# Kernel optimization log

Measured on AMD Instinct MI355X. Metric: run time of the kernel, lower is better.

Reference implementation:

```python
import jax, jax.numpy as jnp
import numpy as np
from jax import lax

DN = ('NCHW', 'OIHW', 'NCHW')

def _conv(x, w, b):
    y = lax.conv_general_dilated(x, w, (1, 1), 'SAME', dimension_numbers=DN)
    return y + b[None, :, None, None]

def setup_inputs() -> dict:
    key = jax.random.key(0)
    ks = jax.random.split(key, 12)
    B, C, H, W = 8, 32, 128, 128
    Cb, INT, K, FK = 64, 64, 3, 3
    inp = {
        'z': jax.random.normal(ks[0], (B, C, H, W), jnp.float32),
        'backbone': jax.random.normal(ks[1], (B, Cb, H, W), jnp.float32),
        'mem_stab': jax.random.normal(ks[2], (B, C, H, W), jnp.float32),
        'mem_unstab': jax.random.normal(ks[3], (B, C, H, W), jnp.float32),
        'w0': jax.random.normal(ks[4], (INT, Cb + 3 * C, K, K), jnp.float32) * 0.05,
        'b0': jnp.zeros((INT,), jnp.float32),
        'w1': jax.random.normal(ks[5], (INT, INT, K, K), jnp.float32) * 0.05,
        'b1': jnp.zeros((INT,), jnp.float32),
        'w2': jax.random.normal(ks[6], (INT, INT, K, K), jnp.float32) * 0.05,
        'b2': jnp.zeros((INT,), jnp.float32),
        'w_last': jax.random.normal(ks[7], (C * FK * FK, INT, K, K), jnp.float32) * 0.05,
        'b_last': jnp.full((C * FK * FK,), -4.0, jnp.float32),
        'fusion_kernel_size': FK,
    }
    return inp

def reference(z, backbone, mem_stab, mem_unstab, w0, b0, w1, b1, w2, b2, w_last, b_last, fusion_kernel_size):
    B, C, H, W = z.shape
    k = int(fusion_kernel_size)
    p = k * k
    # controller conv stack (LeakyReLU slope 0.01, matching nn.LeakyReLU default)
    q = jnp.concatenate([backbone, z, mem_stab, mem_unstab], axis=1)
    q = jax.nn.leaky_relu(_conv(q, w0, b0), 0.01)
    q = jax.nn.leaky_relu(_conv(q, w1, b1), 0.01)
    q = jax.nn.leaky_relu(_conv(q, w2, b2), 0.01)
    # fusion head -> [B, C, p, HW]
    head = _conv(q, w_last, b_last).reshape(B, C, p, H * W)
    # softmax over p kernel positions + one extra logit-0 slot for z itself
    eta = jax.nn.softmax(jnp.concatenate([head, jnp.zeros_like(head[:, :, :1])], axis=2), axis=2)
    # unfold(mem_stab, k, padding=k//2): patches ordered (c, kh, kw) like torch unfold
    pad = k // 2
    mpad = jnp.pad(mem_stab, ((0, 0), (0, 0), (pad, pad), (pad, pad)))
    patches = jnp.stack([mpad[:, :, i:i + H, j:j + W] for i in range(k) for j in range(k)], axis=2)
    patches = patches.reshape(B, C, p, H * W)
    z_flat = z.reshape(B, C, H * W)
    z_stab = (patches * eta[:, :, :p]).sum(axis=2) + eta[:, :, p] * z_flat
    return z_stab.reshape(B, C, H, W)
```

## Files before the change

kernel.cpp:

```cpp
#include <hip/hip_runtime.h>
#include <hip/hip_fp16.h>

typedef _Float16 half8 __attribute__((ext_vector_type(8)));
typedef _Float16 half4v __attribute__((ext_vector_type(4)));
typedef float floatx4 __attribute__((ext_vector_type(4)));

#define HW 128
#define IMG (HW * HW)
#define PH 130
#define WP 200

typedef __attribute__((address_space(3))) _Float16 lds_f16;
typedef __attribute__((address_space(1))) const _Float16 glb_f16;
__device__ __forceinline__ void gload16(const _Float16* g, _Float16* l) {
    __builtin_amdgcn_global_load_lds((glb_f16*)g, (lds_f16*)l, 16, 0, 0);
}

__global__ void pack_w_all(const float* __restrict__ w0, const float* __restrict__ w1,
                           const float* __restrict__ w2, const float* __restrict__ wl,
                           _Float16* __restrict__ p0, _Float16* __restrict__ p1,
                           _Float16* __restrict__ p2, _Float16* __restrict__ pl) {
    int idx = blockIdx.x * 256 + threadIdx.x;
    const float* w; _Float16* p; int C; int local;
    if (idx < 92160)       { w = w0; p = p0; C = 160; local = idx; }
    else if (idx < 129024) { w = w1; p = p1; C = 64;  local = idx - 92160; }
    else if (idx < 165888) { w = w2; p = p2; C = 64;  local = idx - 129024; }
    else if (idx < 331776) { w = wl; p = pl; C = 64;  local = idx - 165888; }
    else return;
    int o = local / (C * 9);
    int rem = local % (C * 9);
    int c = rem / 9;
    int t = rem % 9;
    p[(o * 9 + t) * C + c] = (_Float16)w[local];
}

__device__ __forceinline__ void zero_halo(_Float16* P, int C, int id) {
    int nvec = C / 8;
    int b = id / (516 * nvec);
    int r = id % (516 * nvec);
    int cell = r / nvec;
    int v = r % nvec;
    int hh, ww;
    if (cell < 130)      { hh = 0;   ww = cell; }
    else if (cell < 260) { hh = 129; ww = cell - 130; }
    else if (cell < 388) { hh = cell - 260 + 1; ww = 0; }
    else                 { hh = cell - 388 + 1; ww = 129; }
    half8 z8 = {};
    *reinterpret_cast<half8*>(P + (((size_t)b * PH + hh) * PH + ww) * C + v * 8) = z8;
}

__global__ void zero_pads_pre(_Float16* __restrict__ X0, _Float16* __restrict__ Q1) {
    int id = blockIdx.x * 256 + threadIdx.x;
    if (id < 82560) zero_halo(X0, 160, id);
    else if (id < 115584) zero_halo(Q1, 64, id - 82560);
}

__global__ void zero_pads64(_Float16* __restrict__ P) {
    int id = blockIdx.x * 256 + threadIdx.x;
    if (id < 33024) zero_halo(P, 64, id);
}

__global__ __launch_bounds__(256)
void pack_in(const float* __restrict__ z, const float* __restrict__ bb,
             const float* __restrict__ ms, const float* __restrict__ mu,
             _Float16* __restrict__ X0) {
    __shared__ _Float16 lds[160 * 132];
    int b = blockIdx.x >> 7;
    int h = blockIdx.x & 127;
    int tid = threadIdx.x;

    for (int i = 0; i < 20; i++) {
        int id = i * 256 + tid;
        int c = id >> 5;
        int col = (id & 31) * 4;
        const float* src; int cs; int csz;
        if (c < 64)       { src = bb; cs = c;       csz = 64; }
        else if (c < 96)  { src = z;  cs = c - 64;  csz = 32; }
        else if (c < 128) { src = ms; cs = c - 96;  csz = 32; }
        else              { src = mu; cs = c - 128; csz = 32; }
        float4 v = *reinterpret_cast<const float4*>(
            src + ((size_t)b * csz + cs) * IMG + h * HW + col);
        half4v hv = { (_Float16)v.x, (_Float16)v.y, (_Float16)v.z, (_Float16)v.w };
        *reinterpret_cast<half4v*>(&lds[c * 132 + col]) = hv;
    }
    __syncthreads();
    _Float16* dst = X0 + (((size_t)b * PH + (h + 1)) * PH + 1) * 160;
    for (int i = 0; i < 10; i++) {
        int id = i * 256 + tid;
        int pix = id / 20;
        int c0 = (id % 20) * 8;
        half8 hv;
        #pragma unroll
        for (int e = 0; e < 8; e++) hv[e] = lds[(c0 + e) * 132 + pix];
        *reinterpret_cast<half8*>(dst + (size_t)pix * 160 + c0) = hv;
    }
}

__global__ __launch_bounds__(256, 2)
void conv3_c160(const _Float16* __restrict__ X, const _Float16* __restrict__ Wp,
                const float* __restrict__ bias, _Float16* __restrict__ Y) {
    __shared__ _Float16 xs[130 * 168];
    int b = blockIdx.x >> 7;
    int h = blockIdx.x & 127;
    int tid = threadIdx.x;
    int lane = tid & 63;
    int wave = tid >> 6;
    int ph = wave & 1;
    int oh = wave >> 1;
    int l15 = lane & 15;
    int l4  = lane >> 4;

    floatx4 acc[4][2] = {};
    half8 SA[10], SB[10];

    const _Float16* wl = Wp + (size_t)((oh * 32 + l15) * 9) * 160 + l4 * 8;

#define LOADW(S, k) { \
    _Pragma("unroll") \
    for (int cb = 0; cb < 5; cb++) \
      _Pragma("unroll") \
      for (int n = 0; n < 2; n++) \
        S[cb * 2 + n] = *reinterpret_cast<const half8*>( \
            wl + n * 23040 + (k) * 160 + cb * 32); }

#define STAGE160(r) { \
    const _Float16* grow = X + ((size_t)b * PH + (h + (r))) * PH * 160; \
    _Pragma("unroll") \
    for (int i = 0; i < 11; i++) { \
      int id = i * 256 + tid; \
      if (id < 2600) { \
        half8 v = *reinterpret_cast<const half8*>(grow + (size_t)id * 8); \
        *reinterpret_cast<half8*>(&xs[(id / 20) * 168 + (id % 20) * 8]) = v; \
      } } }

#define COMP160(dw, S) { \
    _Pragma("unroll") \
    for (int cb = 0; cb < 5; cb++) { \
      int kofs = cb * 32 + l4 * 8; \
      half8 af[4]; \
      _Pragma("unroll") \
      for (int m = 0; m < 4; m++) { \
        int p = ph * 64 + m * 16 + l15; \
        af[m] = *reinterpret_cast<const half8*>(&xs[(p + (dw)) * 168 + kofs]); \
      } \
      _Pragma("unroll") \
      for (int m = 0; m < 4; m++) \
        _Pragma("unroll") \
        for (int n = 0; n < 2; n++) \
          acc[m][n] = __builtin_amdgcn_mfma_f32_16x16x32_f16( \
              af[m], S[cb * 2 + n], acc[m][n], 0, 0, 0); } }

    LOADW(SA, 0);
    STAGE160(0);
    __syncthreads();
    LOADW(SB, 1);  COMP160(0, SA);
    LOADW(SA, 2);  COMP160(1, SB);
    LOADW(SB, 3);  COMP160(2, SA);
    __syncthreads();
    STAGE160(1);
    __syncthreads();
    LOADW(SA, 4);  COMP160(0, SB);
    LOADW(SB, 5);  COMP160(1, SA);
    LOADW(SA, 6);  COMP160(2, SB);
    __syncthreads();
    STAGE160(2);
    __syncthreads();
    LOADW(SB, 7);  COMP160(0, SA);
    LOADW(SA, 8);  COMP160(1, SB);
    COMP160(2, SA);

#undef LOADW
#undef STAGE160
#undef COMP160

    _Float16* dst = Y + (((size_t)b * PH + (h + 1)) * PH + 1) * 64;
    #pragma unroll
    for (int m = 0; m < 4; m++)
        #pragma unroll
        for (int n = 0; n < 2; n++) {
            int o = oh * 32 + n * 16 + l15;
            float bv = bias[o];
            #pragma unroll
            for (int q = 0; q < 4; q++) {
                int pix = ph * 64 + m * 16 + l4 * 4 + q;
                float v = acc[m][n][q] + bv;
                v = v > 0.f ? v : 0.01f * v;
                dst[(size_t)pix * 64 + o] = (_Float16)v;
            }
        }
}

__global__ __launch_bounds__(256, 3)
void conv3_c64(const _Float16* __restrict__ X, const _Float16* __restrict__ Wp,
               const float* __restrict__ bias, _Float16* __restrict__ Y) {
    __shared__ _Float16 smem[9360 + 64 * WP];
    _Float16* xs = smem;
    _Float16* wbuf = smem + 9360;
    int b = blockIdx.x >> 7;
    int h = blockIdx.x & 127;
    int tid = threadIdx.x;
    int lane = tid & 63;
    int wave = tid >> 6;
    int ph = wave & 1;
    int oh = wave >> 1;
    int l15 = lane & 15;
    int l4  = lane >> 4;

    floatx4 acc[4][2] = {};
    const _Float16* xbase = X + ((size_t)b * PH + h) * (PH * 64);

    for (int r = 0; r < 3; r++) {
        if (r) __syncthreads();
        for (int i = 0; i < 5; i++) {
            int id = i * 256 + tid;
            if (id < 1040) {
                half8 v = *reinterpret_cast<const half8*>(
                    xbase + (size_t)r * (PH * 64) + (size_t)id * 8);
                *reinterpret_cast<half8*>(&xs[(id >> 3) * 72 + (id & 7) * 8]) = v;
            }
        }
        for (int i = 0; i < 6; i++) {
            int id = i * 256 + tid;
            int o = id / 24, j = id % 24;
            half8 v = *reinterpret_cast<const half8*>(
                Wp + ((size_t)o * 9 + r * 3) * 64 + j * 8);
            *reinterpret_cast<half8*>(&wbuf[o * WP + j * 8]) = v;
        }
        __syncthreads();
        #pragma unroll
        for (int dw = 0; dw < 3; dw++)
            #pragma unroll
            for (int cb = 0; cb < 2; cb++) {
                int kofs = cb * 32 + l4 * 8;
                half8 bf[2];
                #pragma unroll
                for (int n = 0; n < 2; n++) {
                    int o = oh * 32 + n * 16 + l15;
                    bf[n] = *reinterpret_cast<const half8*>(
                        &wbuf[o * WP + dw * 64 + kofs]);
                }
                half8 af[4];
                #pragma unroll
                for (int m = 0; m < 4; m++) {
                    int p = ph * 64 + m * 16 + l15;
                    af[m] = *reinterpret_cast<const half8*>(&xs[(p + dw) * 72 + kofs]);
                }
                #pragma unroll
                for (int m = 0; m < 4; m++)
                    #pragma unroll
                    for (int n = 0; n < 2; n++)
                        acc[m][n] = __builtin_amdgcn_mfma_f32_16x16x32_f16(
                            af[m], bf[n], acc[m][n], 0, 0, 0);
            }
    }
    _Float16* dst = Y + (((size_t)b * PH + (h + 1)) * PH + 1) * 64;
    #pragma unroll
    for (int m = 0; m < 4; m++)
        #pragma unroll
        for (int n = 0; n < 2; n++) {
            int o = oh * 32 + n * 16 + l15;
            float bv = bias[o];
            #pragma unroll
            for (int q = 0; q < 4; q++) {
                int pix = ph * 64 + m * 16 + l4 * 4 + q;
                float v = acc[m][n][q] + bv;
                v = v > 0.f ? v : 0.01f * v;
                dst[(size_t)pix * 64 + o] = (_Float16)v;
            }
        }
}

__global__ __launch_bounds__(256, 3)
void head_gemm(const _Float16* __restrict__ X, const _Float16* __restrict__ Wp,
               const float* __restrict__ b_last, _Float16* __restrict__ Lg,
               int bbase) {
    __shared__ _Float16 smem[26752];
    _Float16* xs = smem;
    _Float16* wbuf = smem + 8320;
    _Float16* tb = smem;
    int blk = blockIdx.x;
    int ct = blk >> 9;
    int bi = (blk >> 7) & 3;
    int h  = blk & 127;
    int b = bbase + bi;
    int tid = threadIdx.x;
    int lane = tid & 63;
    int wave = tid >> 6;
    int pxh = wave & 1;
    int og  = wave >> 1;
    int l15 = lane & 15;
    int l4  = lane >> 4;

    floatx4 acc[4][3] = {};
    const _Float16* xbase = X + ((size_t)b * PH + h) * (PH * 64);
    const _Float16* wbase = Wp + (size_t)ct * 96 * 9 * 64;

    for (int r = 0; r < 3; r++) {
        if (r) __syncthreads();
        const _Float16* xrow = xbase + (size_t)r * (PH * 64);
        for (int i = 0; i < 5; i++) {
            int sbase = i * 256 + wave * 64;
            int s = sbase + lane;
            if (s < 1040) {
                int px = s >> 3;
                int j = (s & 7) ^ (px & 7);
                gload16(xrow + (size_t)(px * 8 + j) * 8, xs + (size_t)sbase * 8);
            }
        }
        const _Float16* wrow = wbase + r * 192;
        for (int i = 0; i < 9; i++) {
            int tbs = i * 256 + wave * 64;
            int t = tbs + lane;
            int o = t / 24, ks = t % 24;
            int k = (ks & 0x18) | ((ks & 7) ^ (o & 7));
            gload16(wrow + (size_t)(o * 576 + k * 8), wbuf + (size_t)tbs * 8);
        }
        __syncthreads();
        #pragma unroll
        for (int dw = 0; dw < 3; dw++)
            #pragma unroll
            for (int cb = 0; cb < 2; cb++) {
                int kb = dw * 8 + cb * 4 + l4;
                half8 bf[3];
                #pragma unroll
                for (int n = 0; n < 3; n++) {
                    int ol = og * 48 + n * 16 + l15;
                    int ksw = (kb & 0x18) | ((kb & 7) ^ (ol & 7));
                    bf[n] = *reinterpret_cast<const half8*>(&wbuf[ol * 192 + ksw * 8]);
                }
                int j = cb * 4 + l4;
                half8 af[4];
                #pragma unroll
                for (int m = 0; m < 4; m++) {
                    int px = pxh * 64 + m * 16 + l15 + dw;
                    af[m] = *reinterpret_cast<const half8*>(
                        &xs[px * 64 + (j ^ (px & 7)) * 8]);
                }
                #pragma unroll
                for (int m = 0; m < 4; m++)
                    #pragma unroll
                    for (int n = 0; n < 3; n++)
                        acc[m][n] = __builtin_amdgcn_mfma_f32_16x16x32_f16(
                            af[m], bf[n], acc[m][n], 0, 0, 0);
            }
    }
    __syncthreads();

    #pragma unroll
    for (int m = 0; m < 4; m++)
        #pragma unroll
        for (int n = 0; n < 3; n++) {
            int od = og * 48 + n * 16 + l15;
            float bv = b_last[ct * 96 + od];
            half4v hv;
            #pragma unroll
            for (int q = 0; q < 4; q++) hv[q] = (_Float16)(acc[m][n][q] + bv);
            *reinterpret_cast<half4v*>(&tb[od * 132 + pxh * 64 + m * 16 + l4 * 4]) = hv;
        }
    __syncthreads();

    _Float16* dst = Lg + (((size_t)bi * 128 + h) * 288 + (size_t)ct * 96) * 128;
    #pragma unroll
    for (int i = 0; i < 6; i++) {
        int id = i * 256 + tid;
        int od = id >> 4;
        int sl = id & 15;
        half8 v = *reinterpret_cast<const half8*>(&tb[od * 132 + sl * 8]);
        *reinterpret_cast<half8*>(dst + (size_t)od * 128 + sl * 8) = v;
    }
}

__global__ __launch_bounds__(256)
void fuse_sm(const _Float16* __restrict__ Lg, const float* __restrict__ ms,
             const float* __restrict__ zin, float* __restrict__ out, int bbase) {
    int blk = blockIdx.x;
    int bi = blk >> 11;
    int c  = (blk >> 6) & 31;
    int hp = blk & 63;
    int tid = threadIdx.x;
    int h = hp * 2 + (tid >> 7);
    int w = tid & 127;
    int b = bbase + bi;

    const _Float16* lrow = Lg + (((size_t)bi * 128 + h) * 288 + (size_t)c * 9) * 128 + w;
    float L[9];
    float mx = 0.f;
    #pragma unroll
    for (int j = 0; j < 9; j++) { L[j] = (float)lrow[j * 128]; mx = fmaxf(mx, L[j]); }
    float ez = __expf(-mx);
    float sum = ez;
    float e[9];
    #pragma unroll
    for (int j = 0; j < 9; j++) { e[j] = __expf(L[j] - mx); sum += e[j]; }
    float inv = 1.f / sum;
    const float* msb = ms + ((size_t)b * 32 + c) * IMG;
    float accv = ez * inv * zin[((size_t)b * 32 + c) * IMG + h * HW + w];
    #pragma unroll
    for (int kh = 0; kh < 3; kh++) {
        int h2 = h + kh - 1;
        int h2c = min(max(h2, 0), 127);
        bool okh = (unsigned)h2 < 128u;
        #pragma unroll
        for (int kw = 0; kw < 3; kw++) {
            int w2 = w + kw - 1;
            int w2c = min(max(w2, 0), 127);
            bool okw = (unsigned)w2 < 128u;
            float mv = msb[h2c * HW + w2c];
            accv += e[kh * 3 + kw] * inv * ((okh && okw) ? mv : 0.f);
        }
    }
    out[((size_t)b * 32 + c) * IMG + h * HW + w] = accv;
}

extern "C" void kernel_launch(void* const* d_in, const int* in_sizes, int n_in,
                              void* d_out, int out_size, void* d_ws, size_t ws_size,
                              hipStream_t stream) {
    const float* z  = (const float*)d_in[0];
    const float* bb = (const float*)d_in[1];
    const float* ms = (const float*)d_in[2];
    const float* mu = (const float*)d_in[3];
    const float* w0 = (const float*)d_in[4];
    const float* b0 = (const float*)d_in[5];
    const float* w1 = (const float*)d_in[6];
    const float* b1 = (const float*)d_in[7];
    const float* w2 = (const float*)d_in[8];
    const float* b2 = (const float*)d_in[9];
    const float* wl = (const float*)d_in[10];
    const float* bl = (const float*)d_in[11];

    char* ws = (char*)d_ws;
    _Float16* Wp0 = (_Float16*)(ws + 0);
    _Float16* Wp1 = (_Float16*)(ws + 184320);
    _Float16* Wp2 = (_Float16*)(ws + 258048);
    _Float16* WpL = (_Float16*)(ws + 331776);
    _Float16* BufA = (_Float16*)(ws + 663552);
    _Float16* BufB = (_Float16*)(ws + 43927552);

    _Float16* X0 = BufA;
    _Float16* Q1 = BufB;
    _Float16* Q2 = BufA;
    _Float16* Q3 = BufB;
    _Float16* Lg = BufA;

    pack_w_all<<<(331776 + 255) / 256, 256, 0, stream>>>(w0, w1, w2, wl, Wp0, Wp1, Wp2, WpL);
    zero_pads_pre<<<(115584 + 255) / 256, 256, 0, stream>>>(X0, Q1);
    pack_in<<<1024, 256, 0, stream>>>(z, bb, ms, mu, X0);

    conv3_c160<<<1024, 256, 0, stream>>>(X0, Wp0, b0, Q1);
    zero_pads64<<<(33024 + 255) / 256, 256, 0, stream>>>(Q2);
    conv3_c64<<<1024, 256, 0, stream>>>(Q1, Wp1, b1, Q2);
    conv3_c64<<<1024, 256, 0, stream>>>(Q2, Wp2, b2, Q3);

    head_gemm<<<1536, 256, 0, stream>>>(Q3, WpL, bl, Lg, 0);
    fuse_sm<<<8192, 256, 0, stream>>>(Lg, ms, z, (float*)d_out, 0);
    head_gemm<<<1536, 256, 0, stream>>>(Q3, WpL, bl, Lg, 4);
    fuse_sm<<<8192, 256, 0, stream>>>(Lg, ms, z, (float*)d_out, 4);
}
```

Measured before the change: 196.3 us.

## Split first conv into half-row blocks with double-buffered LDS staging

The first 160-channel conv now gives each block half an output row (64 pixels), so the grid doubles to 2048 blocks and each block holds half the accumulators. The LDS tile shrinks to two 66-pixel buffers, which allows double buffering: the next input row is staged while the current one is computed, removing the stage-then-sync bubbles. Occupancy hint rises from 2 to 3 blocks per CU. The cost is that each weight load is now amortized over half as many pixels, so weight traffic per output roughly doubles.

Result: slower. 212.0 us (+8.0%).

```diff
diff --git a/kernel.cpp b/kernel.cpp
--- a/kernel.cpp
+++ b/kernel.cpp
@@ -96,12 +96,14 @@
     }
 }
 
-__global__ __launch_bounds__(256, 2)
+__global__ __launch_bounds__(256, 3)
 void conv3_c160(const _Float16* __restrict__ X, const _Float16* __restrict__ Wp,
                 const float* __restrict__ bias, _Float16* __restrict__ Y) {
-    __shared__ _Float16 xs[130 * 168];
-    int b = blockIdx.x >> 7;
-    int h = blockIdx.x & 127;
+    __shared__ _Float16 xs[2][66 * 168];
+    int blk = blockIdx.x;
+    int b = blk >> 8;
+    int h = (blk >> 1) & 127;
+    int wb64 = (blk & 1) * 64;
     int tid = threadIdx.x;
     int lane = tid & 63;
     int wave = tid >> 6;
@@ -110,7 +112,7 @@
     int l15 = lane & 15;
     int l4  = lane >> 4;
 
-    floatx4 acc[4][2] = {};
+    floatx4 acc[2][2] = {};
     half8 SA[10], SB[10];
 
     const _Float16* wl = Wp + (size_t)((oh * 32 + l15) * 9) * 160 + l4 * 8;
@@ -123,66 +125,64 @@
         S[cb * 2 + n] = *reinterpret_cast<const half8*>( \
             wl + n * 23040 + (k) * 160 + cb * 32); }
 
-#define STAGE160(r) { \
-    const _Float16* grow = X + ((size_t)b * PH + (h + (r))) * PH * 160; \
+#define STAGE160(BUF, r) { \
+    const _Float16* grow = X + (((size_t)b * PH + (h + (r))) * PH + wb64) * 160; \
     _Pragma("unroll") \
-    for (int i = 0; i < 11; i++) { \
+    for (int i = 0; i < 6; i++) { \
       int id = i * 256 + tid; \
-      if (id < 2600) { \
+      if (id < 1320) { \
         half8 v = *reinterpret_cast<const half8*>(grow + (size_t)id * 8); \
-        *reinterpret_cast<half8*>(&xs[(id / 20) * 168 + (id % 20) * 8]) = v; \
+        *reinterpret_cast<half8*>(&BUF[(id / 20) * 168 + (id % 20) * 8]) = v; \
       } } }
 
-#define COMP160(dw, S) { \
+#define COMP160(dw, S, BUF) { \
     _Pragma("unroll") \
     for (int cb = 0; cb < 5; cb++) { \
       int kofs = cb * 32 + l4 * 8; \
-      half8 af[4]; \
+      half8 af[2]; \
       _Pragma("unroll") \
-      for (int m = 0; m < 4; m++) { \
-        int p = ph * 64 + m * 16 + l15; \
-        af[m] = *reinterpret_cast<const half8*>(&xs[(p + (dw)) * 168 + kofs]); \
+      for (int m = 0; m < 2; m++) { \
+        int p = ph * 32 + m * 16 + l15; \
+        af[m] = *reinterpret_cast<const half8*>(&BUF[(p + (dw)) * 168 + kofs]); \
       } \
       _Pragma("unroll") \
-      for (int m = 0; m < 4; m++) \
+      for (int m = 0; m < 2; m++) \
         _Pragma("unroll") \
         for (int n = 0; n < 2; n++) \
           acc[m][n] = __builtin_amdgcn_mfma_f32_16x16x32_f16( \
               af[m], S[cb * 2 + n], acc[m][n], 0, 0, 0); } }
 
     LOADW(SA, 0);
-    STAGE160(0);
-    __syncthreads();
-    LOADW(SB, 1);  COMP160(0, SA);
-    LOADW(SA, 2);  COMP160(1, SB);
-    LOADW(SB, 3);  COMP160(2, SA);
-    __syncthreads();
-    STAGE160(1);
-    __syncthreads();
-    LOADW(SA, 4);  COMP160(0, SB);
-    LOADW(SB, 5);  COMP160(1, SA);
-    LOADW(SA, 6);  COMP160(2, SB);
-    __syncthreads();
-    STAGE160(2);
-    __syncthreads();
-    LOADW(SB, 7);  COMP160(0, SA);
-    LOADW(SA, 8);  COMP160(1, SB);
-    COMP160(2, SA);
+    STAGE160(xs[0], 0);
+    __syncthreads();
+    STAGE160(xs[1], 1);
+    LOADW(SB, 1);  COMP160(0, SA, xs[0]);
+    LOADW(SA, 2);  COMP160(1, SB, xs[0]);
+    LOADW(SB, 3);  COMP160(2, SA, xs[0]);
+    __syncthreads();
+    STAGE160(xs[0], 2);
+    LOADW(SA, 4);  COMP160(0, SB, xs[1]);
+    LOADW(SB, 5);  COMP160(1, SA, xs[1]);
+    LOADW(SA, 6);  COMP160(2, SB, xs[1]);
+    __syncthreads();
+    LOADW(SB, 7);  COMP160(0, SA, xs[0]);
+    LOADW(SA, 8);  COMP160(1, SB, xs[0]);
+    COMP160(2, SA, xs[0]);
 
 #undef LOADW
 #undef STAGE160
 #undef COMP160
 
-    _Float16* dst = Y + (((size_t)b * PH + (h + 1)) * PH + 1) * 64;
-    #pragma unroll
-    for (int m = 0; m < 4; m++)
+    _Float16* dst = Y + (((size_t)b * PH + (h + 1)) * PH + 1 + wb64) * 64;
+    #pragma unroll
+    for (int m = 0; m < 2; m++)
         #pragma unroll
         for (int n = 0; n < 2; n++) {
             int o = oh * 32 + n * 16 + l15;
             float bv = bias[o];
             #pragma unroll
             for (int q = 0; q < 4; q++) {
-                int pix = ph * 64 + m * 16 + l4 * 4 + q;
+                int pix = ph * 32 + m * 16 + l4 * 4 + q;
                 float v = acc[m][n][q] + bv;
                 v = v > 0.f ? v : 0.01f * v;
                 dst[(size_t)pix * 64 + o] = (_Float16)v;
@@ -446,7 +446,7 @@
     zero_pads_pre<<<(115584 + 255) / 256, 256, 0, stream>>>(X0, Q1);
     pack_in<<<1024, 256, 0, stream>>>(z, bb, ms, mu, X0);
 
-    conv3_c160<<<1024, 256, 0, stream>>>(X0, Wp0, b0, Q1);
+    conv3_c160<<<2048, 256, 0, stream>>>(X0, Wp0, b0, Q1);
     zero_pads64<<<(33024 + 255) / 256, 256, 0, stream>>>(Q2);
     conv3_c64<<<1024, 256, 0, stream>>>(Q1, Wp1, b1, Q2);
     conv3_c64<<<1024, 256, 0, stream>>>(Q2, Wp2, b2, Q3);
```
